# Optimization experiments

Hardware: AMD Instinct MI355X
Metric: run time of the kernel (lower is better)

Reference implementation:

```python
import jax, jax.numpy as jnp
import numpy as np

N = 50000      # nodes
E = 300000     # edges
F_IN = 128     # num_features
H = 256        # hidden_dim
C = 32         # num_classes


def gcn_conv(x, src, dst, W, b, num_nodes):
    """PyG-style GCNConv: add self-loops, sym-normalize, X W, scatter-add, + bias."""
    loop = jnp.arange(num_nodes, dtype=src.dtype)
    src2 = jnp.concatenate([src, loop])          # [E+N]
    dst2 = jnp.concatenate([dst, loop])          # [E+N]
    # degree of target nodes (with self-loops, unit edge weights)
    deg = jax.ops.segment_sum(jnp.ones_like(dst2, dtype=x.dtype), dst2,
                              num_segments=num_nodes)
    dinv = jnp.where(deg > 0, jax.lax.rsqrt(deg), 0.0)
    norm = dinv[src2] * dinv[dst2]               # [E+N]
    h = x @ W                                    # [N, out]  dense GEMM first (PyG order)
    msg = h[src2] * norm[:, None]                # gather + scale  [E+N, out]
    out = jax.ops.segment_sum(msg, dst2, num_segments=num_nodes)  # scatter-add
    return out + b


def setup_inputs() -> dict:
    key = jax.random.key(0)
    ks = jax.random.split(key, 8)
    x = jax.random.normal(ks[0], (N, F_IN), dtype=jnp.float32)
    edge_index = jax.random.randint(ks[1], (2, E), 0, N, dtype=jnp.int64)
    W1 = jax.random.normal(ks[2], (F_IN, H), dtype=jnp.float32) / np.float32(np.sqrt(F_IN))
    b1 = jnp.zeros((H,), jnp.float32)
    W2 = jax.random.normal(ks[3], (H, H), dtype=jnp.float32) / np.float32(np.sqrt(H))
    b2 = jnp.zeros((H,), jnp.float32)
    Wc = jax.random.normal(ks[4], (H, C), dtype=jnp.float32) / np.float32(np.sqrt(H))
    bc = jnp.zeros((C,), jnp.float32)
    return {"x": x, "edge_index": edge_index, "W1": W1, "b1": b1,
            "W2": W2, "b2": b2, "Wc": Wc, "bc": bc}


def reference(x, edge_index, W1, b1, W2, b2, Wc, bc):
    src, dst = edge_index[0], edge_index[1]
    h = gcn_conv(x, src, dst, W1, b1, N)
    h = jax.nn.relu(h)                 # dropout is identity in eval mode
    h = gcn_conv(h, src, dst, W2, b2, N)
    h = jax.nn.relu(h)
    return h @ Wc + bc                 # [N, C]
```

## Files before the change

### kernel.cpp

```cpp
#include <hip/hip_runtime.h>
#include <math.h>

using short8 = __attribute__((ext_vector_type(8))) short;
using f32x4 = __attribute__((ext_vector_type(4))) float;

#define CAP 48

__device__ inline short f2bf(float f) {
    unsigned u = __builtin_bit_cast(unsigned, f);
    unsigned r = (u + 0x7fffu + ((u >> 16) & 1u)) >> 16;
    return (short)r;
}
__device__ inline float bf2f(short s) {
    unsigned u = ((unsigned)(unsigned short)s) << 16;
    return __builtin_bit_cast(float, u);
}


__global__ void prep_kernel(const float* __restrict__ x, const float* __restrict__ W1,
                            const float* __restrict__ W2, const float* __restrict__ Wc,
                            const int* __restrict__ src, const int* __restrict__ dst,
                            short* __restrict__ xb, short* __restrict__ Wt1,
                            short* __restrict__ Wt2, short* __restrict__ Wtc,
                            int* __restrict__ deg, int* __restrict__ eslot,
                            int n, int e) {
    int idx = blockIdx.x * blockDim.x + threadIdx.x;
    const int nx8 = n * 16;
    if (idx < nx8) {
        const float4* p = (const float4*)x + (size_t)idx * 2;
        float4 v0 = p[0], v1 = p[1];
        short8 o;
        o[0] = f2bf(v0.x); o[1] = f2bf(v0.y); o[2] = f2bf(v0.z); o[3] = f2bf(v0.w);
        o[4] = f2bf(v1.x); o[5] = f2bf(v1.y); o[6] = f2bf(v1.z); o[7] = f2bf(v1.w);
        ((short8*)xb)[idx] = o;
        return;
    }
    idx -= nx8;
    if (idx < 128 * 256) {
        int k = idx >> 8, c = idx & 255;
        Wt1[c * 128 + k] = f2bf(W1[idx]);
        return;
    }
    idx -= 128 * 256;
    if (idx < 256 * 256) {
        int k = idx >> 8, c = idx & 255;
        Wt2[c * 256 + k] = f2bf(W2[idx]);
        return;
    }
    idx -= 256 * 256;
    if (idx < 256 * 32) {
        int k = idx >> 5, c = idx & 31;
        Wtc[c * 256 + k] = f2bf(Wc[idx]);
        return;
    }
    idx -= 256 * 32;
    if (idx < e) {
        int d = dst[idx], s = src[idx];
        int pos = atomicAdd(&deg[d], 1);
        if (pos < CAP) eslot[(size_t)d * CAP + pos] = s;
    }
}


template<bool RELU_BF16OUT>
__global__ __launch_bounds__(256) void mfma_gemm128_kernel(
    const short* __restrict__ A, const short* __restrict__ Wt,
    const float* __restrict__ bias, void* __restrict__ Cout,
    int M, int K, int NC)
{
    __shared__ short As[128 * 40];
    __shared__ short Bs[128 * 40];

    const int tid = threadIdx.x;
    const int wave = tid >> 6, lane = tid & 63;
    const int m0 = blockIdx.y * 128, n0 = blockIdx.x * 128;
    const int wm = (wave >> 1) * 64, wn = (wave & 1) * 64;

    const int sar = tid >> 2;
    const int sak = (tid & 3) * 8;
    int ga0 = m0 + sar;      if (ga0 >= M) ga0 = M - 1;
    int ga1 = m0 + 64 + sar; if (ga1 >= M) ga1 = M - 1;
    int gb0 = n0 + sar;      if (gb0 >= NC) gb0 = NC - 1;
    int gb1 = n0 + 64 + sar; if (gb1 >= NC) gb1 = NC - 1;
    const short* pa0 = A + (size_t)ga0 * K + sak;
    const short* pa1 = A + (size_t)ga1 * K + sak;
    const short* pb0 = Wt + (size_t)gb0 * K + sak;
    const short* pb1 = Wt + (size_t)gb1 * K + sak;

    const int lw0 = sar * 40 + sak;
    const int lw1 = (64 + sar) * 40 + sak;

    f32x4 acc[4][4] = {};
    const int fr = lane & 15;
    const int fk = (lane >> 4) * 8;

    for (int k0 = 0; k0 < K; k0 += 32) {
        short8 va0 = *(const short8*)(pa0 + k0);
        short8 va1 = *(const short8*)(pa1 + k0);
        short8 vb0 = *(const short8*)(pb0 + k0);
        short8 vb1 = *(const short8*)(pb1 + k0);
        __syncthreads();
        *(short8*)&As[lw0] = va0;
        *(short8*)&As[lw1] = va1;
        *(short8*)&Bs[lw0] = vb0;
        *(short8*)&Bs[lw1] = vb1;
        __syncthreads();

        short8 af[4], bfv[4];
        #pragma unroll
        for (int mt = 0; mt < 4; ++mt)
            af[mt] = *(const short8*)&As[(wm + mt * 16 + fr) * 40 + fk];
        #pragma unroll
        for (int nt = 0; nt < 4; ++nt)
            bfv[nt] = *(const short8*)&Bs[(wn + nt * 16 + fr) * 40 + fk];

        #pragma unroll
        for (int mt = 0; mt < 4; ++mt)
            #pragma unroll
            for (int nt = 0; nt < 4; ++nt)
                acc[mt][nt] = __builtin_amdgcn_mfma_f32_16x16x32_bf16(
                    af[mt], bfv[nt], acc[mt][nt], 0, 0, 0);
    }

    #pragma unroll
    for (int mt = 0; mt < 4; ++mt) {
        #pragma unroll
        for (int nt = 0; nt < 4; ++nt) {
            #pragma unroll
            for (int r = 0; r < 4; ++r) {
                int grow = m0 + wm + mt * 16 + (lane >> 4) * 4 + r;
                int gcol = n0 + wn + nt * 16 + (lane & 15);
                if (grow < M && gcol < NC) {
                    float v = acc[mt][nt][r] + bias[gcol];
                    if (RELU_BF16OUT)
                        ((short*)Cout)[(size_t)grow * NC + gcol] = f2bf(fmaxf(v, 0.f));
                    else
                        ((float*)Cout)[(size_t)grow * NC + gcol] = v;
                }
            }
        }
    }
}


__global__ __launch_bounds__(128) void mfma_gemmc_kernel(
    const short* __restrict__ A, const short* __restrict__ Wt,
    const float* __restrict__ bias, float* __restrict__ Cout,
    int M, int K)
{
    const int NC = 32;
    __shared__ short As[128 * 40];
    __shared__ short Bs[32 * 40];

    const int tid = threadIdx.x;
    const int wave = tid >> 6, lane = tid & 63;
    const int m0 = blockIdx.x * 128;
    const int wm = wave * 64;

    const int sar = tid >> 2;
    const int sak = (tid & 3) * 8;
    int gr0 = m0 + sar;       if (gr0 >= M) gr0 = M - 1;
    int gr1 = m0 + 32 + sar;  if (gr1 >= M) gr1 = M - 1;
    int gr2 = m0 + 64 + sar;  if (gr2 >= M) gr2 = M - 1;
    int gr3 = m0 + 96 + sar;  if (gr3 >= M) gr3 = M - 1;
    const short* pa0 = A + (size_t)gr0 * K + sak;
    const short* pa1 = A + (size_t)gr1 * K + sak;
    const short* pa2 = A + (size_t)gr2 * K + sak;
    const short* pa3 = A + (size_t)gr3 * K + sak;
    const short* pb  = Wt + (size_t)sar * K + sak;

    f32x4 acc[4][2] = {};
    const int fr = lane & 15;
    const int fk = (lane >> 4) * 8;

    for (int k0 = 0; k0 < K; k0 += 32) {
        short8 va0 = *(const short8*)(pa0 + k0);
        short8 va1 = *(const short8*)(pa1 + k0);
        short8 va2 = *(const short8*)(pa2 + k0);
        short8 va3 = *(const short8*)(pa3 + k0);
        short8 vb  = *(const short8*)(pb + k0);
        __syncthreads();
        *(short8*)&As[(sar)       * 40 + sak] = va0;
        *(short8*)&As[(32 + sar)  * 40 + sak] = va1;
        *(short8*)&As[(64 + sar)  * 40 + sak] = va2;
        *(short8*)&As[(96 + sar)  * 40 + sak] = va3;
        *(short8*)&Bs[sar * 40 + sak] = vb;
        __syncthreads();

        short8 af[4], bfv[2];
        #pragma unroll
        for (int mt = 0; mt < 4; ++mt)
            af[mt] = *(const short8*)&As[(wm + mt * 16 + fr) * 40 + fk];
        #pragma unroll
        for (int nt = 0; nt < 2; ++nt)
            bfv[nt] = *(const short8*)&Bs[(nt * 16 + fr) * 40 + fk];

        #pragma unroll
        for (int mt = 0; mt < 4; ++mt)
            #pragma unroll
            for (int nt = 0; nt < 2; ++nt)
                acc[mt][nt] = __builtin_amdgcn_mfma_f32_16x16x32_bf16(
                    af[mt], bfv[nt], acc[mt][nt], 0, 0, 0);
    }

    #pragma unroll
    for (int mt = 0; mt < 4; ++mt) {
        #pragma unroll
        for (int nt = 0; nt < 2; ++nt) {
            #pragma unroll
            for (int r = 0; r < 4; ++r) {
                int grow = m0 + wm + mt * 16 + (lane >> 4) * 4 + r;
                int gcol = nt * 16 + (lane & 15);
                if (grow < M)
                    Cout[(size_t)grow * NC + gcol] = acc[mt][nt][r] + bias[gcol];
            }
        }
    }
}


template<int LPN>
__global__ __launch_bounds__(256) void gather_kernel(
    const short* __restrict__ h, const int* __restrict__ deg,
    const int* __restrict__ eslot, short* __restrict__ out, int n)
{
    const int F = LPN * 8;
    int node = (blockIdx.x * 256 + threadIdx.x) / LPN;
    if (node >= n) return;
    int lane = threadIdx.x % LPN;
    int f = lane * 8;

    int dg = deg[node];
    if (dg > CAP) dg = CAP;
    float di = rsqrtf((float)dg + 1.0f);
    float w = di * di;

    const size_t rb = (size_t)node * F + f;
    short8 hv = *(const short8*)(h + rb);
    float a[8];
    #pragma unroll
    for (int j = 0; j < 8; ++j) a[j] = bf2f(hv[j]) * w;

    const int* bucket = eslot + (size_t)node * CAP;
    for (int e = 0; e < dg; e += 4) {
        int4 s4 = *(const int4*)(bucket + e);
        int i0 = s4.x;
        int i1 = (e + 1 < dg) ? s4.y : 0;
        int i2 = (e + 2 < dg) ? s4.z : 0;
        int i3 = (e + 3 < dg) ? s4.w : 0;
        int d0 = deg[i0], d1 = deg[i1], d2 = deg[i2], d3 = deg[i3];
        short8 v0 = *(const short8*)(h + (size_t)i0 * F + f);
        short8 v1 = *(const short8*)(h + (size_t)i1 * F + f);
        short8 v2 = *(const short8*)(h + (size_t)i2 * F + f);
        short8 v3 = *(const short8*)(h + (size_t)i3 * F + f);
        float w0 = rsqrtf((float)d0 + 1.0f) * di;
        float w1 = (e + 1 < dg) ? rsqrtf((float)d1 + 1.0f) * di : 0.f;
        float w2 = (e + 2 < dg) ? rsqrtf((float)d2 + 1.0f) * di : 0.f;
        float w3 = (e + 3 < dg) ? rsqrtf((float)d3 + 1.0f) * di : 0.f;
        #pragma unroll
        for (int j = 0; j < 8; ++j) {
            a[j] = fmaf(bf2f(v0[j]), w0, a[j]);
            a[j] = fmaf(bf2f(v1[j]), w1, a[j]);
            a[j] = fmaf(bf2f(v2[j]), w2, a[j]);
            a[j] = fmaf(bf2f(v3[j]), w3, a[j]);
        }
    }
    short8 o;
    #pragma unroll
    for (int j = 0; j < 8; ++j) o[j] = f2bf(a[j]);
    *(short8*)(out + rb) = o;
}


extern "C" void kernel_launch(void* const* d_in, const int* in_sizes, int n_in,
                              void* d_out, int out_size, void* d_ws, size_t ws_size,
                              hipStream_t stream) {
    const float* x  = (const float*)d_in[0];
    const int*   ei = (const int*)d_in[1];
    const float* W1 = (const float*)d_in[2];
    const float* b1 = (const float*)d_in[3];
    const float* W2 = (const float*)d_in[4];
    const float* b2 = (const float*)d_in[5];
    const float* Wc = (const float*)d_in[6];
    const float* bc = (const float*)d_in[7];
    float* out = (float*)d_out;

    const int E = in_sizes[1] / 2;
    const int N = in_sizes[0] / 128;
    const int F_IN = 128, H = 256;
    const int* src = ei;
    const int* dst = ei + E;

    short* xb   = (short*)d_ws;
    short* aggX = xb + (size_t)N * 128;
    short* hA   = aggX + (size_t)N * 128;
    short* hB   = hA + (size_t)N * 256;
    short* Wt1  = hB + (size_t)N * 256;
    short* Wt2  = Wt1 + 256 * 128;
    short* Wtc  = Wt2 + 256 * 256;
    int*   deg  = (int*)(Wtc + 32 * 256);
    int*   eslot= deg + N;

    const int TB = 256;

    hipMemsetAsync(deg, 0, (size_t)N * sizeof(int), stream);

    const int prep_total = N * 16 + 128 * 256 + 256 * 256 + 256 * 32 + E;
    prep_kernel<<<(prep_total + TB - 1) / TB, TB, 0, stream>>>(
        x, W1, W2, Wc, src, dst, xb, Wt1, Wt2, Wtc, deg, eslot, N, E);

    const int gy = (N + 127) / 128;

    gather_kernel<16><<<((size_t)N * 16 + TB - 1) / TB, TB, 0, stream>>>(
        xb, deg, eslot, aggX, N);
    mfma_gemm128_kernel<true><<<dim3(H / 128, gy), 256, 0, stream>>>(aggX, Wt1, b1, hA, N, F_IN, H);

    gather_kernel<32><<<((size_t)N * 32 + TB - 1) / TB, TB, 0, stream>>>(
        hA, deg, eslot, hB, N);
    mfma_gemm128_kernel<true><<<dim3(H / 128, gy), 256, 0, stream>>>(hB, Wt2, b2, hA, N, H, H);

    mfma_gemmc_kernel<<<gy, 128, 0, stream>>>(hA, Wtc, bc, out, N, H);
}
```

Baseline: 221.0 us.

## Prescale layer-1 output by dinv and widen gather unroll to eight neighbors

The first GEMM epilogue now multiplies each output row by that node's inverse square-root degree. The second-layer gather can therefore sum neighbor rows without a per-edge degree lookup and rsqrt, applying the destination scale once at the end. The gather loop also issues eight neighbor row loads per iteration instead of four, for more memory-level parallelism. The cost is more registers in the gather, and rows are now rounded to bf16 after scaling, which changes rounding slightly.

```diff
diff --git a/kernel.cpp b/kernel.cpp
--- a/kernel.cpp
+++ b/kernel.cpp
@@ -62,10 +62,11 @@
 }
 
 
-template<bool RELU_BF16OUT>
+template<bool RELU_BF16OUT, bool SCALE_DINV>
 __global__ __launch_bounds__(256) void mfma_gemm128_kernel(
     const short* __restrict__ A, const short* __restrict__ Wt,
     const float* __restrict__ bias, void* __restrict__ Cout,
+    const int* __restrict__ deg,
     int M, int K, int NC)
 {
     __shared__ short As[128 * 40];
@@ -125,15 +126,20 @@
     #pragma unroll
     for (int mt = 0; mt < 4; ++mt) {
         #pragma unroll
-        for (int nt = 0; nt < 4; ++nt) {
-            #pragma unroll
-            for (int r = 0; r < 4; ++r) {
-                int grow = m0 + wm + mt * 16 + (lane >> 4) * 4 + r;
+        for (int r = 0; r < 4; ++r) {
+            int grow = m0 + wm + mt * 16 + (lane >> 4) * 4 + r;
+            if (grow >= M) continue;
+            float rowscale = 1.0f;
+            if (SCALE_DINV)
+                rowscale = rsqrtf((float)deg[grow] + 1.0f);
+            #pragma unroll
+            for (int nt = 0; nt < 4; ++nt) {
                 int gcol = n0 + wn + nt * 16 + (lane & 15);
-                if (grow < M && gcol < NC) {
+                if (gcol < NC) {
                     float v = acc[mt][nt][r] + bias[gcol];
                     if (RELU_BF16OUT)
-                        ((short*)Cout)[(size_t)grow * NC + gcol] = f2bf(fmaxf(v, 0.f));
+                        ((short*)Cout)[(size_t)grow * NC + gcol] =
+                            f2bf(fmaxf(v, 0.f) * rowscale);
                     else
                         ((float*)Cout)[(size_t)grow * NC + gcol] = v;
                 }
@@ -219,7 +225,7 @@
 }
 
 
-template<int LPN>
+template<int LPN, bool PRESCALED>
 __global__ __launch_bounds__(256) void gather_kernel(
     const short* __restrict__ h, const int* __restrict__ deg,
     const int* __restrict__ eslot, short* __restrict__ out, int n)
@@ -233,38 +239,58 @@
     int dg = deg[node];
     if (dg > CAP) dg = CAP;
     float di = rsqrtf((float)dg + 1.0f);
-    float w = di * di;
 
     const size_t rb = (size_t)node * F + f;
     short8 hv = *(const short8*)(h + rb);
     float a[8];
+    const float selfw = PRESCALED ? 1.0f : di * di;
     #pragma unroll
-    for (int j = 0; j < 8; ++j) a[j] = bf2f(hv[j]) * w;
+    for (int j = 0; j < 8; ++j) a[j] = bf2f(hv[j]) * selfw;
 
     const int* bucket = eslot + (size_t)node * CAP;
-    for (int e = 0; e < dg; e += 4) {
-        int4 s4 = *(const int4*)(bucket + e);
-        int i0 = s4.x;
-        int i1 = (e + 1 < dg) ? s4.y : 0;
-        int i2 = (e + 2 < dg) ? s4.z : 0;
-        int i3 = (e + 3 < dg) ? s4.w : 0;
-        int d0 = deg[i0], d1 = deg[i1], d2 = deg[i2], d3 = deg[i3];
-        short8 v0 = *(const short8*)(h + (size_t)i0 * F + f);
-        short8 v1 = *(const short8*)(h + (size_t)i1 * F + f);
-        short8 v2 = *(const short8*)(h + (size_t)i2 * F + f);
-        short8 v3 = *(const short8*)(h + (size_t)i3 * F + f);
-        float w0 = rsqrtf((float)d0 + 1.0f) * di;
-        float w1 = (e + 1 < dg) ? rsqrtf((float)d1 + 1.0f) * di : 0.f;
-        float w2 = (e + 2 < dg) ? rsqrtf((float)d2 + 1.0f) * di : 0.f;
-        float w3 = (e + 3 < dg) ? rsqrtf((float)d3 + 1.0f) * di : 0.f;
-        #pragma unroll
-        for (int j = 0; j < 8; ++j) {
-            a[j] = fmaf(bf2f(v0[j]), w0, a[j]);
-            a[j] = fmaf(bf2f(v1[j]), w1, a[j]);
-            a[j] = fmaf(bf2f(v2[j]), w2, a[j]);
-            a[j] = fmaf(bf2f(v3[j]), w3, a[j]);
+    for (int e = 0; e < dg; e += 8) {
+        int4 sa = *(const int4*)(bucket + e);
+        int4 sb = *(const int4*)(bucket + e + 4);
+        int id[8];
+        id[0] = sa.x;
+        id[1] = (e + 1 < dg) ? sa.y : 0;
+        id[2] = (e + 2 < dg) ? sa.z : 0;
+        id[3] = (e + 3 < dg) ? sa.w : 0;
+        id[4] = (e + 4 < dg) ? sb.x : 0;
+        id[5] = (e + 5 < dg) ? sb.y : 0;
+        id[6] = (e + 6 < dg) ? sb.z : 0;
+        id[7] = (e + 7 < dg) ? sb.w : 0;
+
+        short8 v[8];
+        #pragma unroll
+        for (int t = 0; t < 8; ++t)
+            v[t] = *(const short8*)(h + (size_t)id[t] * F + f);
+
+        float w[8];
+        if (PRESCALED) {
+            #pragma unroll
+            for (int t = 0; t < 8; ++t)
+                w[t] = (e + t < dg) ? 1.0f : 0.0f;
+        } else {
+            #pragma unroll
+            for (int t = 0; t < 8; ++t) {
+                float ds = (float)deg[id[t]];
+                w[t] = (e + t < dg) ? rsqrtf(ds + 1.0f) * di : 0.0f;
+            }
         }
-    }
+
+        #pragma unroll
+        for (int t = 0; t < 8; ++t)
+            #pragma unroll
+            for (int j = 0; j < 8; ++j)
+                a[j] = fmaf(bf2f(v[t][j]), w[t], a[j]);
+    }
+
+    if (PRESCALED) {
+        #pragma unroll
+        for (int j = 0; j < 8; ++j) a[j] *= di;
+    }
+
     short8 o;
     #pragma unroll
     for (int j = 0; j < 8; ++j) o[j] = f2bf(a[j]);
@@ -311,13 +337,15 @@
 
     const int gy = (N + 127) / 128;
 
-    gather_kernel<16><<<((size_t)N * 16 + TB - 1) / TB, TB, 0, stream>>>(
+    gather_kernel<16, false><<<((size_t)N * 16 + TB - 1) / TB, TB, 0, stream>>>(
         xb, deg, eslot, aggX, N);
-    mfma_gemm128_kernel<true><<<dim3(H / 128, gy), 256, 0, stream>>>(aggX, Wt1, b1, hA, N, F_IN, H);
-
-    gather_kernel<32><<<((size_t)N * 32 + TB - 1) / TB, TB, 0, stream>>>(
+    mfma_gemm128_kernel<true, true><<<dim3(H / 128, gy), 256, 0, stream>>>(
+        aggX, Wt1, b1, hA, deg, N, F_IN, H);
+
+    gather_kernel<32, true><<<((size_t)N * 32 + TB - 1) / TB, TB, 0, stream>>>(
         hA, deg, eslot, hB, N);
-    mfma_gemm128_kernel<true><<<dim3(H / 128, gy), 256, 0, stream>>>(hB, Wt2, b2, hA, N, H, H);
+    mfma_gemm128_kernel<true, false><<<dim3(H / 128, gy), 256, 0, stream>>>(
+        hB, Wt2, b2, hA, deg, N, H, H);
 
     mfma_gemmc_kernel<<<gy, 128, 0, stream>>>(hA, Wtc, bc, out, N, H);
 }
```

Result: slower. 238.4 us (+7.9%).

## Precompute degree normalization table and fold source scaling into GEMM epilogue

Applied to the files above, without the earlier changes.

Adds a small kernel that computes 1/sqrt(deg+1) per node once into a float table. The first GEMM's epilogue now multiplies its ReLU output rows by this factor, so the second gather can sum neighbor rows with unit weights and apply only the destination factor at the end. The first gather reads the table instead of loading deg and computing rsqrt per edge. The memset now also zeroes the edge-slot buckets so padded lanes read node 0, which adds a larger memset and an extra launch; the pre-scaled bf16 storage also slightly changes rounding.

```diff
diff --git a/kernel.cpp b/kernel.cpp
--- a/kernel.cpp
+++ b/kernel.cpp
@@ -62,10 +62,17 @@
 }
 
 
-template<bool RELU_BF16OUT>
+__global__ void dinv_kernel(const int* __restrict__ deg, float* __restrict__ dinvt, int n) {
+    int i = blockIdx.x * blockDim.x + threadIdx.x;
+    if (i < n) dinvt[i] = rsqrtf((float)deg[i] + 1.0f);
+}
+
+
+template<bool RELU_BF16OUT, bool SCALE_DINV>
 __global__ __launch_bounds__(256) void mfma_gemm128_kernel(
     const short* __restrict__ A, const short* __restrict__ Wt,
     const float* __restrict__ bias, void* __restrict__ Cout,
+    const float* __restrict__ dinvt,
     int M, int K, int NC)
 {
     __shared__ short As[128 * 40];
@@ -125,15 +132,20 @@
     #pragma unroll
     for (int mt = 0; mt < 4; ++mt) {
         #pragma unroll
-        for (int nt = 0; nt < 4; ++nt) {
+        for (int r = 0; r < 4; ++r) {
+            int grow = m0 + wm + mt * 16 + (lane >> 4) * 4 + r;
+            if (grow >= M) continue;
+            float rowscale = 1.0f;
+            if (SCALE_DINV)
+                rowscale = dinvt[grow];
             #pragma unroll
-            for (int r = 0; r < 4; ++r) {
-                int grow = m0 + wm + mt * 16 + (lane >> 4) * 4 + r;
+            for (int nt = 0; nt < 4; ++nt) {
                 int gcol = n0 + wn + nt * 16 + (lane & 15);
-                if (grow < M && gcol < NC) {
+                if (gcol < NC) {
                     float v = acc[mt][nt][r] + bias[gcol];
                     if (RELU_BF16OUT)
-                        ((short*)Cout)[(size_t)grow * NC + gcol] = f2bf(fmaxf(v, 0.f));
+                        ((short*)Cout)[(size_t)grow * NC + gcol] =
+                            f2bf(fmaxf(v, 0.f) * rowscale);
                     else
                         ((float*)Cout)[(size_t)grow * NC + gcol] = v;
                 }
@@ -219,10 +231,11 @@
 }
 
 
-template<int LPN>
+template<int LPN, bool PRESCALED>
 __global__ __launch_bounds__(256) void gather_kernel(
     const short* __restrict__ h, const int* __restrict__ deg,
-    const int* __restrict__ eslot, short* __restrict__ out, int n)
+    const float* __restrict__ dinvt, const int* __restrict__ eslot,
+    short* __restrict__ out, int n)
 {
     const int F = LPN * 8;
     int node = (blockIdx.x * 256 + threadIdx.x) / LPN;
@@ -232,31 +245,30 @@
 
     int dg = deg[node];
     if (dg > CAP) dg = CAP;
-    float di = rsqrtf((float)dg + 1.0f);
-    float w = di * di;
 
     const size_t rb = (size_t)node * F + f;
     short8 hv = *(const short8*)(h + rb);
-    float a[8];
-    #pragma unroll
-    for (int j = 0; j < 8; ++j) a[j] = bf2f(hv[j]) * w;
+    float a[8] = {};
 
     const int* bucket = eslot + (size_t)node * CAP;
     for (int e = 0; e < dg; e += 4) {
         int4 s4 = *(const int4*)(bucket + e);
-        int i0 = s4.x;
-        int i1 = (e + 1 < dg) ? s4.y : 0;
-        int i2 = (e + 2 < dg) ? s4.z : 0;
-        int i3 = (e + 3 < dg) ? s4.w : 0;
-        int d0 = deg[i0], d1 = deg[i1], d2 = deg[i2], d3 = deg[i3];
-        short8 v0 = *(const short8*)(h + (size_t)i0 * F + f);
-        short8 v1 = *(const short8*)(h + (size_t)i1 * F + f);
-        short8 v2 = *(const short8*)(h + (size_t)i2 * F + f);
-        short8 v3 = *(const short8*)(h + (size_t)i3 * F + f);
-        float w0 = rsqrtf((float)d0 + 1.0f) * di;
-        float w1 = (e + 1 < dg) ? rsqrtf((float)d1 + 1.0f) * di : 0.f;
-        float w2 = (e + 2 < dg) ? rsqrtf((float)d2 + 1.0f) * di : 0.f;
-        float w3 = (e + 3 < dg) ? rsqrtf((float)d3 + 1.0f) * di : 0.f;
+        short8 v0 = *(const short8*)(h + (size_t)s4.x * F + f);
+        short8 v1 = *(const short8*)(h + (size_t)s4.y * F + f);
+        short8 v2 = *(const short8*)(h + (size_t)s4.z * F + f);
+        short8 v3 = *(const short8*)(h + (size_t)s4.w * F + f);
+        float w0, w1, w2, w3;
+        if (PRESCALED) {
+            w0 = 1.0f;
+            w1 = (e + 1 < dg) ? 1.0f : 0.0f;
+            w2 = (e + 2 < dg) ? 1.0f : 0.0f;
+            w3 = (e + 3 < dg) ? 1.0f : 0.0f;
+        } else {
+            w0 = dinvt[s4.x];
+            w1 = (e + 1 < dg) ? dinvt[s4.y] : 0.0f;
+            w2 = (e + 2 < dg) ? dinvt[s4.z] : 0.0f;
+            w3 = (e + 3 < dg) ? dinvt[s4.w] : 0.0f;
+        }
         #pragma unroll
         for (int j = 0; j < 8; ++j) {
             a[j] = fmaf(bf2f(v0[j]), w0, a[j]);
@@ -265,9 +277,13 @@
             a[j] = fmaf(bf2f(v3[j]), w3, a[j]);
         }
     }
+
+    float di = rsqrtf((float)dg + 1.0f);
+    const float selfw = PRESCALED ? 1.0f : di;
     short8 o;
     #pragma unroll
-    for (int j = 0; j < 8; ++j) o[j] = f2bf(a[j]);
+    for (int j = 0; j < 8; ++j)
+        o[j] = f2bf(fmaf(bf2f(hv[j]), selfw, a[j]) * di);
     *(short8*)(out + rb) = o;
 }
 
@@ -300,24 +316,29 @@
     short* Wtc  = Wt2 + 256 * 256;
     int*   deg  = (int*)(Wtc + 32 * 256);
     int*   eslot= deg + N;
+    float* dinvt= (float*)(eslot + (size_t)N * CAP);
 
     const int TB = 256;
 
-    hipMemsetAsync(deg, 0, (size_t)N * sizeof(int), stream);
+    hipMemsetAsync(deg, 0, (size_t)N * (CAP + 1) * sizeof(int), stream);
 
     const int prep_total = N * 16 + 128 * 256 + 256 * 256 + 256 * 32 + E;
     prep_kernel<<<(prep_total + TB - 1) / TB, TB, 0, stream>>>(
         x, W1, W2, Wc, src, dst, xb, Wt1, Wt2, Wtc, deg, eslot, N, E);
 
+    dinv_kernel<<<(N + TB - 1) / TB, TB, 0, stream>>>(deg, dinvt, N);
+
     const int gy = (N + 127) / 128;
 
-    gather_kernel<16><<<((size_t)N * 16 + TB - 1) / TB, TB, 0, stream>>>(
-        xb, deg, eslot, aggX, N);
-    mfma_gemm128_kernel<true><<<dim3(H / 128, gy), 256, 0, stream>>>(aggX, Wt1, b1, hA, N, F_IN, H);
-
-    gather_kernel<32><<<((size_t)N * 32 + TB - 1) / TB, TB, 0, stream>>>(
-        hA, deg, eslot, hB, N);
-    mfma_gemm128_kernel<true><<<dim3(H / 128, gy), 256, 0, stream>>>(hB, Wt2, b2, hA, N, H, H);
+    gather_kernel<16, false><<<((size_t)N * 16 + TB - 1) / TB, TB, 0, stream>>>(
+        xb, deg, dinvt, eslot, aggX, N);
+    mfma_gemm128_kernel<true, true><<<dim3(H / 128, gy), 256, 0, stream>>>(
+        aggX, Wt1, b1, hA, dinvt, N, F_IN, H);
+
+    gather_kernel<32, true><<<((size_t)N * 32 + TB - 1) / TB, TB, 0, stream>>>(
+        hA, deg, dinvt, eslot, hB, N);
+    mfma_gemm128_kernel<true, false><<<dim3(H / 128, gy), 256, 0, stream>>>(
+        hB, Wt2, b2, hA, dinvt, N, H, H);
 
     mfma_gemmc_kernel<<<gy, 128, 0, stream>>>(hA, Wtc, bc, out, N, H);
 }
```

Result: slower. 230.0 us (+4.1%).
